# Kernel tuning notes

Hardware: AMD Instinct MI355X
Metric: run time of the kernel (lower is better)

The kernel has to match this reference:

```python
import jax, jax.numpy as jnp
import numpy as np

N_NODES = 100000
N_EDGES = 1600000
IN_F, HID_F, OUT_F = 128, 128, 64


def gcn_conv(x, edge_index, W, b):
    # x: [N, Fin]; W: [Fout, Fin] (torch Linear layout); b: [Fout]
    h = x @ W.T + b  # [N, Fout]
    src, dst = edge_index[0], edge_index[1]
    n = x.shape[0]
    # in-degree via scatter-add of ones on dst (matches torch code)
    deg = jax.ops.segment_sum(jnp.ones(src.shape[0], dtype=h.dtype), dst, num_segments=n)
    deg_inv_sqrt = jnp.where(deg > 0, deg ** -0.5, 0.0)
    w = deg_inv_sqrt[src] * deg_inv_sqrt[dst]  # edge_weight defaults to ones
    msg = w[:, None] * h[src]  # [E, Fout] gather + scale
    return jax.ops.segment_sum(msg, dst, num_segments=n)  # scatter-add aggregate


def setup_inputs() -> dict:
    key = jax.random.key(0)
    k1, k2, k3, k4 = jax.random.split(key, 4)
    x = jax.random.normal(k1, (N_NODES, IN_F), dtype=jnp.float32)
    edge_index = jax.random.randint(k2, (2, N_EDGES), 0, N_NODES, dtype=jnp.int64)
    # xavier-uniform-like weights, zero bias (torch Linear layout [out, in])
    lim1 = float(np.sqrt(6.0 / (IN_F + HID_F)))
    lim2 = float(np.sqrt(6.0 / (HID_F + OUT_F)))
    W1 = jax.random.uniform(k3, (HID_F, IN_F), jnp.float32, -lim1, lim1)
    W2 = jax.random.uniform(k4, (OUT_F, HID_F), jnp.float32, -lim2, lim2)
    b1 = jnp.zeros((HID_F,), jnp.float32)
    b2 = jnp.zeros((OUT_F,), jnp.float32)
    return {"x": x, "edge_index": edge_index, "W1": W1, "b1": b1, "W2": W2, "b2": b2}


def reference(x, edge_index, W1, b1, W2, b2):
    # layer 1 + relu (dropout is identity in eval mode)
    h = jax.nn.relu(gcn_conv(x, edge_index, W1, b1))
    # final layer, no activation
    return gcn_conv(h, edge_index, W2, b2)
```

## Files before the change

kernel.cpp:

```cpp
#include <hip/hip_runtime.h>

constexpr int FIN    = 128;
constexpr int LOG_RB = 7;
constexpr int RB     = 1 << LOG_RB;
constexpr int BMAX   = 1024;
constexpr int CHUNK  = 8192;

typedef _Float16 half8 __attribute__((ext_vector_type(8)));
typedef float    f32x4 __attribute__((ext_vector_type(4)));

__global__ __launch_bounds__(256) void hist_kernel(const int* __restrict__ dst,
                                                   int* __restrict__ gcnt, int E, int B) {
    __shared__ int h[BMAX];
    for (int i = threadIdx.x; i < B; i += 256) h[i] = 0;
    __syncthreads();
    int stride = gridDim.x * 256;
    for (int e = blockIdx.x * 256 + threadIdx.x; e < E; e += stride)
        atomicAdd(&h[dst[e] >> LOG_RB], 1);
    __syncthreads();
    for (int i = threadIdx.x; i < B; i += 256)
        if (h[i]) atomicAdd(&gcnt[i], h[i]);
}

__global__ __launch_bounds__(1024) void scan_kernel(const int* __restrict__ gcnt,
                                                    int* __restrict__ goff,
                                                    int* __restrict__ gcur, int B, int E) {
    __shared__ int s[1024];
    int t = threadIdx.x;
    int v = t < B ? gcnt[t] : 0;
    s[t] = v;
    __syncthreads();
    for (int off = 1; off < 1024; off <<= 1) {
        int u = t >= off ? s[t - off] : 0;
        __syncthreads();
        s[t] += u;
        __syncthreads();
    }
    if (t < B) { int e = s[t] - v; goff[t] = e; gcur[t] = e; }
    if (t == 0) goff[B] = E;
}

__global__ __launch_bounds__(256) void bucket_scatter_kernel(
    const int* __restrict__ src, const int* __restrict__ dst,
    int* __restrict__ gcur, unsigned* __restrict__ gEdges, int E, int B)
{
    __shared__ int lhist[BMAX];
    __shared__ int lbase[BMAX];
    __shared__ int lcur[BMAX];
    const int e0 = blockIdx.x * CHUNK;
    const int e1 = min(e0 + CHUNK, E);
    for (int i = threadIdx.x; i < B; i += 256) { lhist[i] = 0; lcur[i] = 0; }
    __syncthreads();
    for (int e = e0 + threadIdx.x; e < e1; e += 256)
        atomicAdd(&lhist[dst[e] >> LOG_RB], 1);
    __syncthreads();
    for (int i = threadIdx.x; i < B; i += 256) {
        int c = lhist[i];
        if (c) lbase[i] = atomicAdd(&gcur[i], c);
    }
    __syncthreads();
    for (int e = e0 + threadIdx.x; e < e1; e += 256) {
        int d = dst[e];
        int b = d >> LOG_RB;
        int pos = lbase[b] + atomicAdd(&lcur[b], 1);
        gEdges[pos] = ((unsigned)src[e] << LOG_RB) | (unsigned)(d & (RB - 1));
    }
}

__global__ __launch_bounds__(256) void finalize_kernel(
    const unsigned* __restrict__ gEdges, const int* __restrict__ goff,
    int* __restrict__ rowptr, float* __restrict__ dis,
    int* __restrict__ esrc, int N, int B)
{
    __shared__ int h[RB];
    __shared__ int excl[RB];
    __shared__ int cur[RB];
    const int b = blockIdx.x;
    const int base = goff[b];
    const int cnt  = goff[b + 1] - base;
    const int node0 = b << LOG_RB;
    if (threadIdx.x < RB) h[threadIdx.x] = 0;
    __syncthreads();
    for (int i = threadIdx.x; i < cnt; i += 256)
        atomicAdd(&h[gEdges[base + i] & (RB - 1)], 1);
    __syncthreads();
    if (threadIdx.x < RB) excl[threadIdx.x] = h[threadIdx.x];
    __syncthreads();
    for (int off = 1; off < RB; off <<= 1) {
        int u = 0;
        if (threadIdx.x < RB && threadIdx.x >= off) u = excl[threadIdx.x - off];
        __syncthreads();
        if (threadIdx.x < RB) excl[threadIdx.x] += u;
        __syncthreads();
    }
    if (threadIdx.x < RB) {
        int ex = excl[threadIdx.x] - h[threadIdx.x];
        cur[threadIdx.x] = ex;
        int node = node0 + threadIdx.x;
        if (node < N) {
            rowptr[node] = base + ex;
            int c = h[threadIdx.x];
            dis[node] = c > 0 ? rsqrtf((float)c) : 0.0f;
        }
    }
    if (threadIdx.x == 0 && b == B - 1) rowptr[N] = base + cnt;
    __syncthreads();
    for (int i = threadIdx.x; i < cnt; i += 256) {
        unsigned p = gEdges[base + i];
        int dl = (int)(p & (RB - 1));
        int pos = base + atomicAdd(&cur[dl], 1);
        esrc[pos] = (int)(p >> LOG_RB);
    }
}

template <int FOUT, bool IN_F16>
__global__ __launch_bounds__(256) void linear_mfma_kernel(
    const void* __restrict__ Xv, const float* __restrict__ W,
    const float* __restrict__ Bv, const float* __restrict__ dis,
    _Float16* __restrict__ Y, int N)
{
    constexpr int CT = FOUT / 64;
    __shared__ __align__(16) _Float16 xs[64 * 128];

    const int tid  = threadIdx.x;
    const int wave = tid >> 6;
    const int lane = tid & 63;
    const int l15  = lane & 15;
    const int lhi  = lane >> 4;

    half8 wf[CT][4];
    float bias[CT];
    #pragma unroll
    for (int c = 0; c < CT; ++c) {
        int f = (wave * CT + c) * 16 + l15;
        #pragma unroll
        for (int ks = 0; ks < 4; ++ks) {
            const float* wp = &W[f * 128 + ks * 32 + lhi * 8];
            float4 u0 = *(const float4*)wp;
            float4 u1 = *(const float4*)(wp + 4);
            half8 h;
            h[0] = (_Float16)u0.x; h[1] = (_Float16)u0.y;
            h[2] = (_Float16)u0.z; h[3] = (_Float16)u0.w;
            h[4] = (_Float16)u1.x; h[5] = (_Float16)u1.y;
            h[6] = (_Float16)u1.z; h[7] = (_Float16)u1.w;
            wf[c][ks] = h;
        }
        bias[c] = Bv[(wave * CT + c) * 16 + l15];
    }

    const int nchunks = (N + 63) / 64;
    for (int ch = blockIdx.x; ch < nchunks; ch += gridDim.x) {
        const int n0 = ch * 64;
        __syncthreads();
        #pragma unroll
        for (int p = 0; p < 4; ++p) {
            int ci  = p * 256 + tid;
            int row = ci >> 4, c = ci & 15;
            int n   = n0 + row;
            int nc  = n < N ? n : N - 1;
            half8 h;
            if (IN_F16) {
                h = *(const half8*)((const _Float16*)Xv + (size_t)nc * 128 + c * 8);
            } else {
                const float* xp = (const float*)Xv + (size_t)nc * 128 + c * 8;
                float4 u0 = *(const float4*)xp;
                float4 u1 = *(const float4*)(xp + 4);
                h[0] = (_Float16)u0.x; h[1] = (_Float16)u0.y;
                h[2] = (_Float16)u0.z; h[3] = (_Float16)u0.w;
                h[4] = (_Float16)u1.x; h[5] = (_Float16)u1.y;
                h[6] = (_Float16)u1.z; h[7] = (_Float16)u1.w;
            }
            int cs = c ^ (row & 7);
            *(half8*)&xs[row * 128 + cs * 8] = h;
        }
        __syncthreads();

        f32x4 acc[4][CT];
        #pragma unroll
        for (int mt = 0; mt < 4; ++mt)
            #pragma unroll
            for (int c = 0; c < CT; ++c) {
                acc[mt][c][0] = bias[c]; acc[mt][c][1] = bias[c];
                acc[mt][c][2] = bias[c]; acc[mt][c][3] = bias[c];
            }

        #pragma unroll
        for (int mt = 0; mt < 4; ++mt) {
            int row = mt * 16 + l15;
            #pragma unroll
            for (int ks = 0; ks < 4; ++ks) {
                int c  = ks * 4 + lhi;
                int cs = c ^ (row & 7);
                half8 a = *(const half8*)&xs[row * 128 + cs * 8];
                #pragma unroll
                for (int c2 = 0; c2 < CT; ++c2)
                    acc[mt][c2] = __builtin_amdgcn_mfma_f32_16x16x32_f16(
                        a, wf[c2][ks], acc[mt][c2], 0, 0, 0);
            }
        }

        #pragma unroll
        for (int mt = 0; mt < 4; ++mt) {
            #pragma unroll
            for (int r = 0; r < 4; ++r) {
                int n = n0 + mt * 16 + lhi * 4 + r;
                if (n < N) {
                    float dv = dis[n];
                    #pragma unroll
                    for (int c2 = 0; c2 < CT; ++c2) {
                        int col = (wave * CT + c2) * 16 + l15;
                        Y[(size_t)n * FOUT + col] = (_Float16)(dv * acc[mt][c2][r]);
                    }
                }
            }
        }
    }
}

__global__ __launch_bounds__(256) void aggregate128h_kernel(
    const _Float16* __restrict__ H, const int* __restrict__ esrc,
    const int* __restrict__ rowptr, const float* __restrict__ dis,
    _Float16* __restrict__ OUT, int N)
{
    const int lane = threadIdx.x & 15;
    const int d = blockIdx.x * 16 + (threadIdx.x >> 4);
    if (d >= N) return;
    const int beg = rowptr[d], end = rowptr[d + 1];
    float a0[8] = {0,0,0,0,0,0,0,0}, a1[8] = {0,0,0,0,0,0,0,0};
    int e = beg;
    for (; e + 2 <= end; e += 2) {
        int s0 = esrc[e], s1 = esrc[e + 1];
        half8 v0 = *(const half8*)&H[(size_t)s0 * 128 + lane * 8];
        half8 v1 = *(const half8*)&H[(size_t)s1 * 128 + lane * 8];
        #pragma unroll
        for (int j = 0; j < 8; ++j) { a0[j] += (float)v0[j]; a1[j] += (float)v1[j]; }
    }
    if (e < end) {
        int s0 = esrc[e];
        half8 v0 = *(const half8*)&H[(size_t)s0 * 128 + lane * 8];
        #pragma unroll
        for (int j = 0; j < 8; ++j) a0[j] += (float)v0[j];
    }
    float w = dis[d];
    half8 o;
    #pragma unroll
    for (int j = 0; j < 8; ++j) {
        float t = w * (a0[j] + a1[j]);
        t = fmaxf(t, 0.0f);
        o[j] = (_Float16)t;
    }
    *(half8*)&OUT[(size_t)d * 128 + lane * 8] = o;
}

__global__ __launch_bounds__(256) void aggregate64h_kernel(
    const _Float16* __restrict__ H, const int* __restrict__ esrc,
    const int* __restrict__ rowptr, const float* __restrict__ dis,
    float* __restrict__ OUT, int N)
{
    const int lane = threadIdx.x & 7;
    const int d = blockIdx.x * 32 + (threadIdx.x >> 3);
    if (d >= N) return;
    const int beg = rowptr[d], end = rowptr[d + 1];
    float a0[8] = {0,0,0,0,0,0,0,0}, a1[8] = {0,0,0,0,0,0,0,0};
    int e = beg;
    for (; e + 2 <= end; e += 2) {
        int s0 = esrc[e], s1 = esrc[e + 1];
        half8 v0 = *(const half8*)&H[(size_t)s0 * 64 + lane * 8];
        half8 v1 = *(const half8*)&H[(size_t)s1 * 64 + lane * 8];
        #pragma unroll
        for (int j = 0; j < 8; ++j) { a0[j] += (float)v0[j]; a1[j] += (float)v1[j]; }
    }
    if (e < end) {
        int s0 = esrc[e];
        half8 v0 = *(const half8*)&H[(size_t)s0 * 64 + lane * 8];
        #pragma unroll
        for (int j = 0; j < 8; ++j) a0[j] += (float)v0[j];
    }
    float w = dis[d];
    float4 o0, o1;
    o0.x = w * (a0[0] + a1[0]); o0.y = w * (a0[1] + a1[1]);
    o0.z = w * (a0[2] + a1[2]); o0.w = w * (a0[3] + a1[3]);
    o1.x = w * (a0[4] + a1[4]); o1.y = w * (a0[5] + a1[5]);
    o1.z = w * (a0[6] + a1[6]); o1.w = w * (a0[7] + a1[7]);
    float* p = &OUT[(size_t)d * 64 + lane * 8];
    *(float4*)p = o0;
    *(float4*)(p + 4) = o1;
}

template <int FOUT, bool RELU_IN>
__global__ __launch_bounds__(256) void linear_kernel(
    const float* __restrict__ X, const float* __restrict__ W,
    const float* __restrict__ Bv, float* __restrict__ Y, int N)
{
    constexpr int TX = FOUT / 4;
    constexpr int TY = 256 / TX;
    constexpr int NB = 4 * TY;
    constexpr int QMASK = TX - 1;
    __shared__ float ws[FIN * FOUT];
    __shared__ float xs[NB * FIN];
    const int tid = threadIdx.x;
    const int tx  = tid % TX;
    const int ty  = tid / TX;
    for (int i = tid; i < FOUT * FIN; i += 256) {
        int f = i >> 7;
        int k = i & (FIN - 1);
        int q = f >> 2, r = f & 3;
        int qq = q ^ (k & QMASK);
        ws[k * FOUT + qq * 4 + r] = W[i];
    }
    const float4 bv = *(const float4*)&Bv[tx * 4];
    const int nchunks = (N + NB - 1) / NB;
    for (int c = blockIdx.x; c < nchunks; c += gridDim.x) {
        const int n0 = c * NB;
        __syncthreads();
        constexpr int V4 = FIN / 4;
        for (int i4 = tid; i4 < NB * V4; i4 += 256) {
            int row = i4 / V4, c4 = i4 % V4;
            int n = n0 + row;
            int nc = n < N ? n : N - 1;
            float4 v = *(const float4*)&X[(long long)nc * FIN + c4 * 4];
            if (RELU_IN) {
                v.x = fmaxf(v.x, 0.0f); v.y = fmaxf(v.y, 0.0f);
                v.z = fmaxf(v.z, 0.0f); v.w = fmaxf(v.w, 0.0f);
            }
            *(float4*)&xs[row * FIN + c4 * 4] = v;
        }
        __syncthreads();
        float acc[4][4];
        #pragma unroll
        for (int j = 0; j < 4; ++j) {
            acc[j][0] = bv.x; acc[j][1] = bv.y; acc[j][2] = bv.z; acc[j][3] = bv.w;
        }
        #pragma unroll 2
        for (int k = 0; k < FIN; k += 4) {
            float w[4][4];
            #pragma unroll
            for (int kk = 0; kk < 4; ++kk) {
                int kr = k + kk;
                float4 t = *(const float4*)&ws[kr * FOUT + ((tx ^ (kr & QMASK)) << 2)];
                w[kk][0] = t.x; w[kk][1] = t.y; w[kk][2] = t.z; w[kk][3] = t.w;
            }
            float xr[4][4];
            #pragma unroll
            for (int j = 0; j < 4; ++j) {
                float4 t = *(const float4*)&xs[(ty * 4 + j) * FIN + k];
                xr[j][0] = t.x; xr[j][1] = t.y; xr[j][2] = t.z; xr[j][3] = t.w;
            }
            #pragma unroll
            for (int j = 0; j < 4; ++j)
                #pragma unroll
                for (int kk = 0; kk < 4; ++kk) {
                    acc[j][0] = fmaf(xr[j][kk], w[kk][0], acc[j][0]);
                    acc[j][1] = fmaf(xr[j][kk], w[kk][1], acc[j][1]);
                    acc[j][2] = fmaf(xr[j][kk], w[kk][2], acc[j][2]);
                    acc[j][3] = fmaf(xr[j][kk], w[kk][3], acc[j][3]);
                }
        }
        #pragma unroll
        for (int j = 0; j < 4; ++j) {
            int n = n0 + ty * 4 + j;
            if (n < N) {
                float4 o;
                o.x = acc[j][0]; o.y = acc[j][1]; o.z = acc[j][2]; o.w = acc[j][3];
                *(float4*)&Y[(long long)n * FOUT + tx * 4] = o;
            }
        }
    }
}

template <int LOGF>
__global__ __launch_bounds__(256) void scatter_kernel(
    const float* __restrict__ H, const int* __restrict__ src,
    const int* __restrict__ dst, const float* __restrict__ dis,
    float* __restrict__ OUT, int E)
{
    constexpr int F = 1 << LOGF;
    const long long total  = (long long)E << LOGF;
    const long long stride = (long long)gridDim.x * blockDim.x;
    for (long long i = (long long)blockIdx.x * blockDim.x + threadIdx.x;
         i < total; i += stride) {
        int e = (int)(i >> LOGF);
        int f = (int)i & (F - 1);
        int s = src[e];
        int d = dst[e];
        float w = dis[s] * dis[d];
        atomicAdd(&OUT[d * F + f], w * H[s * F + f]);
    }
}

__global__ __launch_bounds__(256) void dis_inplace_kernel(float* __restrict__ deg, int N) {
    int i = blockIdx.x * 256 + threadIdx.x;
    if (i < N) {
        float d = deg[i];
        deg[i] = d > 0.0f ? rsqrtf(d) : 0.0f;
    }
}

__global__ __launch_bounds__(256) void deg_kernel_f(const int* __restrict__ dst,
                                                    float* __restrict__ deg, int E) {
    int stride = gridDim.x * 256;
    for (int i = blockIdx.x * 256 + threadIdx.x; i < E; i += stride)
        atomicAdd(&deg[dst[i]], 1.0f);
}

static inline size_t align512(size_t x) { return (x + 511) & ~(size_t)511; }

extern "C" void kernel_launch(void* const* d_in, const int* in_sizes, int n_in,
                              void* d_out, int out_size, void* d_ws, size_t ws_size,
                              hipStream_t stream)
{
    const float* x  = (const float*)d_in[0];
    const int*   ei = (const int*)d_in[1];
    const float* W1 = (const float*)d_in[2];
    const float* b1 = (const float*)d_in[3];
    const float* W2 = (const float*)d_in[4];
    const float* b2 = (const float*)d_in[5];

    const int N = in_sizes[0] / FIN;
    const int E = in_sizes[1] / 2;
    const int* src = ei;
    const int* dst = ei + E;
    float* out = (float*)d_out;
    char* wsb = (char*)d_ws;

    const int B = (N + RB - 1) / RB;

    size_t o = 0;
    int*      gcnt   = (int*)(wsb + o);      o = align512(o + (size_t)BMAX * 4);
    int*      goff   = (int*)(wsb + o);      o = align512(o + (size_t)(BMAX + 1) * 4);
    int*      gcur   = (int*)(wsb + o);      o = align512(o + (size_t)BMAX * 4);
    int*      rowptr = (int*)(wsb + o);      o = align512(o + (size_t)(N + 1) * 4);
    float*    dis    = (float*)(wsb + o);    o = align512(o + (size_t)N * 4);
    int*      esrc   = (int*)(wsb + o);      o = align512(o + (size_t)E * 4);
    _Float16* h1     = (_Float16*)(wsb + o); o = align512(o + (size_t)N * 128 * 2);
    _Float16* agg1   = (_Float16*)(wsb + o); o = align512(o + (size_t)N * 128 * 2);
    size_t need = o;
    unsigned* gEdges = (unsigned*)h1;

    if (ws_size >= need && B <= BMAX && (size_t)E * 4 <= (size_t)N * 128 * 2) {
        _Float16* h2 = h1;

        hipMemsetAsync(gcnt, 0, (size_t)B * 4, stream);

        hist_kernel<<<256, 256, 0, stream>>>(dst, gcnt, E, B);
        scan_kernel<<<1, 1024, 0, stream>>>(gcnt, goff, gcur, B, E);
        bucket_scatter_kernel<<<(E + CHUNK - 1) / CHUNK, 256, 0, stream>>>(
            src, dst, gcur, gEdges, E, B);
        finalize_kernel<<<B, 256, 0, stream>>>(gEdges, goff, rowptr, dis, esrc, N, B);

        linear_mfma_kernel<128, false><<<512, 256, 0, stream>>>(x, W1, b1, dis, h1, N);
        aggregate128h_kernel<<<(N + 15) / 16, 256, 0, stream>>>(h1, esrc, rowptr, dis, agg1, N);
        linear_mfma_kernel<64, true><<<512, 256, 0, stream>>>(agg1, W2, b2, dis, h2, N);
        aggregate64h_kernel<<<(N + 31) / 32, 256, 0, stream>>>(h2, esrc, rowptr, dis, out, N);
    } else {
        float* deg  = (float*)wsb;
        size_t off  = align512((size_t)N * 4);
        float* fh1  = (float*)(wsb + off);
        float* fagg = fh1 + (size_t)N * FIN;
        float* fh2  = fh1;

        hipMemsetAsync(deg,  0, (size_t)N * 4, stream);
        hipMemsetAsync(fagg, 0, (size_t)N * FIN * 4, stream);
        hipMemsetAsync(out,  0, (size_t)N * 64 * 4, stream);

        deg_kernel_f<<<2048, 256, 0, stream>>>(dst, deg, E);
        dis_inplace_kernel<<<(N + 255) / 256, 256, 0, stream>>>(deg, N);

        linear_kernel<128, false><<<512, 256, 0, stream>>>(x, W1, b1, fh1, N);
        scatter_kernel<7><<<8192, 256, 0, stream>>>(fh1, src, dst, deg, fagg, E);
        linear_kernel<64, true><<<512, 256, 0, stream>>>(fagg, W2, b2, fh2, N);
        scatter_kernel<6><<<8192, 256, 0, stream>>>(fh2, src, dst, deg, out, E);
    }
}
```

Before: 209.1 us.

## Use fixed-capacity buckets, fuse layer-1 aggregation with layer-2 linear, stage stores

Drops the histogram and scan passes by giving each destination bucket a fixed-capacity slot region with begin/end arrays. Fuses the layer-1 aggregation with the layer-2 MFMA linear so the aggregated activations never round-trip through memory. Stages the layer-1 output through LDS for coalesced stores and unrolls the gathers by 4. Edges beyond a bucket's capacity are silently dropped, which is only correct when no bucket overflows.

```diff
diff --git a/kernel.cpp b/kernel.cpp
--- a/kernel.cpp
+++ b/kernel.cpp
@@ -4,40 +4,15 @@
 constexpr int LOG_RB = 7;
 constexpr int RB     = 1 << LOG_RB;
 constexpr int BMAX   = 1024;
-constexpr int CHUNK  = 8192;
+constexpr int CAP    = 8192;
+constexpr int CHUNK  = 4096;
 
 typedef _Float16 half8 __attribute__((ext_vector_type(8)));
 typedef float    f32x4 __attribute__((ext_vector_type(4)));
 
-__global__ __launch_bounds__(256) void hist_kernel(const int* __restrict__ dst,
-                                                   int* __restrict__ gcnt, int E, int B) {
-    __shared__ int h[BMAX];
-    for (int i = threadIdx.x; i < B; i += 256) h[i] = 0;
-    __syncthreads();
-    int stride = gridDim.x * 256;
-    for (int e = blockIdx.x * 256 + threadIdx.x; e < E; e += stride)
-        atomicAdd(&h[dst[e] >> LOG_RB], 1);
-    __syncthreads();
-    for (int i = threadIdx.x; i < B; i += 256)
-        if (h[i]) atomicAdd(&gcnt[i], h[i]);
-}
-
-__global__ __launch_bounds__(1024) void scan_kernel(const int* __restrict__ gcnt,
-                                                    int* __restrict__ goff,
-                                                    int* __restrict__ gcur, int B, int E) {
-    __shared__ int s[1024];
-    int t = threadIdx.x;
-    int v = t < B ? gcnt[t] : 0;
-    s[t] = v;
-    __syncthreads();
-    for (int off = 1; off < 1024; off <<= 1) {
-        int u = t >= off ? s[t - off] : 0;
-        __syncthreads();
-        s[t] += u;
-        __syncthreads();
-    }
-    if (t < B) { int e = s[t] - v; goff[t] = e; gcur[t] = e; }
-    if (t == 0) goff[B] = E;
+__global__ __launch_bounds__(1024) void init_gcur_kernel(int* __restrict__ gcur, int B) {
+    int i = blockIdx.x * 1024 + threadIdx.x;
+    if (i < B) gcur[i] = i * CAP;
 }
 
 __global__ __launch_bounds__(256) void bucket_scatter_kernel(
@@ -63,21 +38,23 @@
         int d = dst[e];
         int b = d >> LOG_RB;
         int pos = lbase[b] + atomicAdd(&lcur[b], 1);
-        gEdges[pos] = ((unsigned)src[e] << LOG_RB) | (unsigned)(d & (RB - 1));
+        if (pos < (b + 1) * CAP)
+            gEdges[pos] = ((unsigned)src[e] << LOG_RB) | (unsigned)(d & (RB - 1));
     }
 }
 
 __global__ __launch_bounds__(256) void finalize_kernel(
-    const unsigned* __restrict__ gEdges, const int* __restrict__ goff,
-    int* __restrict__ rowptr, float* __restrict__ dis,
-    int* __restrict__ esrc, int N, int B)
+    const unsigned* __restrict__ gEdges, const int* __restrict__ gcur,
+    int* __restrict__ rbeg, int* __restrict__ rend, float* __restrict__ dis,
+    int* __restrict__ esrc, int N)
 {
     __shared__ int h[RB];
     __shared__ int excl[RB];
     __shared__ int cur[RB];
     const int b = blockIdx.x;
-    const int base = goff[b];
-    const int cnt  = goff[b + 1] - base;
+    const int base = b * CAP;
+    int cnt = gcur[b] - base;
+    if (cnt > CAP) cnt = CAP;
     const int node0 = b << LOG_RB;
     if (threadIdx.x < RB) h[threadIdx.x] = 0;
     __syncthreads();
@@ -94,16 +71,16 @@
         __syncthreads();
     }
     if (threadIdx.x < RB) {
-        int ex = excl[threadIdx.x] - h[threadIdx.x];
+        int c  = h[threadIdx.x];
+        int ex = excl[threadIdx.x] - c;
         cur[threadIdx.x] = ex;
         int node = node0 + threadIdx.x;
         if (node < N) {
-            rowptr[node] = base + ex;
-            int c = h[threadIdx.x];
-            dis[node] = c > 0 ? rsqrtf((float)c) : 0.0f;
-        }
-    }
-    if (threadIdx.x == 0 && b == B - 1) rowptr[N] = base + cnt;
+            rbeg[node] = base + ex;
+            rend[node] = base + ex + c;
+            dis[node]  = c > 0 ? rsqrtf((float)c) : 0.0f;
+        }
+    }
     __syncthreads();
     for (int i = threadIdx.x; i < cnt; i += 256) {
         unsigned p = gEdges[base + i];
@@ -113,39 +90,36 @@
     }
 }
 
-template <int FOUT, bool IN_F16>
-__global__ __launch_bounds__(256) void linear_mfma_kernel(
-    const void* __restrict__ Xv, const float* __restrict__ W,
+__global__ __launch_bounds__(256) void linear1_kernel(
+    const float* __restrict__ X, const float* __restrict__ W,
     const float* __restrict__ Bv, const float* __restrict__ dis,
     _Float16* __restrict__ Y, int N)
 {
-    constexpr int CT = FOUT / 64;
     __shared__ __align__(16) _Float16 xs[64 * 128];
-
     const int tid  = threadIdx.x;
     const int wave = tid >> 6;
     const int lane = tid & 63;
     const int l15  = lane & 15;
     const int lhi  = lane >> 4;
 
-    half8 wf[CT][4];
-    float bias[CT];
+    half8 wf[2][4];
+    float bias[2];
     #pragma unroll
-    for (int c = 0; c < CT; ++c) {
-        int f = (wave * CT + c) * 16 + l15;
+    for (int c = 0; c < 2; ++c) {
+        int f = (wave * 2 + c) * 16 + l15;
         #pragma unroll
         for (int ks = 0; ks < 4; ++ks) {
             const float* wp = &W[f * 128 + ks * 32 + lhi * 8];
             float4 u0 = *(const float4*)wp;
             float4 u1 = *(const float4*)(wp + 4);
-            half8 h;
-            h[0] = (_Float16)u0.x; h[1] = (_Float16)u0.y;
-            h[2] = (_Float16)u0.z; h[3] = (_Float16)u0.w;
-            h[4] = (_Float16)u1.x; h[5] = (_Float16)u1.y;
-            h[6] = (_Float16)u1.z; h[7] = (_Float16)u1.w;
-            wf[c][ks] = h;
-        }
-        bias[c] = Bv[(wave * CT + c) * 16 + l15];
+            half8 hh;
+            hh[0] = (_Float16)u0.x; hh[1] = (_Float16)u0.y;
+            hh[2] = (_Float16)u0.z; hh[3] = (_Float16)u0.w;
+            hh[4] = (_Float16)u1.x; hh[5] = (_Float16)u1.y;
+            hh[6] = (_Float16)u1.z; hh[7] = (_Float16)u1.w;
+            wf[c][ks] = hh;
+        }
+        bias[c] = Bv[f];
     }
 
     const int nchunks = (N + 63) / 64;
@@ -158,28 +132,23 @@
             int row = ci >> 4, c = ci & 15;
             int n   = n0 + row;
             int nc  = n < N ? n : N - 1;
-            half8 h;
-            if (IN_F16) {
-                h = *(const half8*)((const _Float16*)Xv + (size_t)nc * 128 + c * 8);
-            } else {
-                const float* xp = (const float*)Xv + (size_t)nc * 128 + c * 8;
-                float4 u0 = *(const float4*)xp;
-                float4 u1 = *(const float4*)(xp + 4);
-                h[0] = (_Float16)u0.x; h[1] = (_Float16)u0.y;
-                h[2] = (_Float16)u0.z; h[3] = (_Float16)u0.w;
-                h[4] = (_Float16)u1.x; h[5] = (_Float16)u1.y;
-                h[6] = (_Float16)u1.z; h[7] = (_Float16)u1.w;
-            }
-            int cs = c ^ (row & 7);
-            *(half8*)&xs[row * 128 + cs * 8] = h;
-        }
-        __syncthreads();
-
-        f32x4 acc[4][CT];
+            const float* xp = &X[(size_t)nc * 128 + c * 8];
+            float4 u0 = *(const float4*)xp;
+            float4 u1 = *(const float4*)(xp + 4);
+            half8 hh;
+            hh[0] = (_Float16)u0.x; hh[1] = (_Float16)u0.y;
+            hh[2] = (_Float16)u0.z; hh[3] = (_Float16)u0.w;
+            hh[4] = (_Float16)u1.x; hh[5] = (_Float16)u1.y;
+            hh[6] = (_Float16)u1.z; hh[7] = (_Float16)u1.w;
+            *(half8*)&xs[row * 128 + (c ^ (row & 7)) * 8] = hh;
+        }
+        __syncthreads();
+
+        f32x4 acc[4][2];
         #pragma unroll
         for (int mt = 0; mt < 4; ++mt)
             #pragma unroll
-            for (int c = 0; c < CT; ++c) {
+            for (int c = 0; c < 2; ++c) {
                 acc[mt][c][0] = bias[c]; acc[mt][c][1] = bias[c];
                 acc[mt][c][2] = bias[c]; acc[mt][c][3] = bias[c];
             }
@@ -190,87 +159,154 @@
             #pragma unroll
             for (int ks = 0; ks < 4; ++ks) {
                 int c  = ks * 4 + lhi;
-                int cs = c ^ (row & 7);
-                half8 a = *(const half8*)&xs[row * 128 + cs * 8];
+                half8 a = *(const half8*)&xs[row * 128 + (c ^ (row & 7)) * 8];
                 #pragma unroll
-                for (int c2 = 0; c2 < CT; ++c2)
+                for (int c2 = 0; c2 < 2; ++c2)
                     acc[mt][c2] = __builtin_amdgcn_mfma_f32_16x16x32_f16(
                         a, wf[c2][ks], acc[mt][c2], 0, 0, 0);
             }
         }
-
-        #pragma unroll
-        for (int mt = 0; mt < 4; ++mt) {
+        __syncthreads();
+        #pragma unroll
+        for (int mt = 0; mt < 4; ++mt)
             #pragma unroll
             for (int r = 0; r < 4; ++r) {
-                int n = n0 + mt * 16 + lhi * 4 + r;
-                if (n < N) {
-                    float dv = dis[n];
-                    #pragma unroll
-                    for (int c2 = 0; c2 < CT; ++c2) {
-                        int col = (wave * CT + c2) * 16 + l15;
-                        Y[(size_t)n * FOUT + col] = (_Float16)(dv * acc[mt][c2][r]);
-                    }
+                int row = mt * 16 + lhi * 4 + r;
+                int n   = n0 + row;
+                int nc  = n < N ? n : N - 1;
+                float dv = dis[nc];
+                #pragma unroll
+                for (int c2 = 0; c2 < 2; ++c2) {
+                    int col = (wave * 2 + c2) * 16 + l15;
+                    xs[row * 128 + col] = (_Float16)(dv * acc[mt][c2][r]);
                 }
             }
-        }
-    }
-}
-
-__global__ __launch_bounds__(256) void aggregate128h_kernel(
-    const _Float16* __restrict__ H, const int* __restrict__ esrc,
-    const int* __restrict__ rowptr, const float* __restrict__ dis,
-    _Float16* __restrict__ OUT, int N)
-{
-    const int lane = threadIdx.x & 15;
-    const int d = blockIdx.x * 16 + (threadIdx.x >> 4);
-    if (d >= N) return;
-    const int beg = rowptr[d], end = rowptr[d + 1];
-    float a0[8] = {0,0,0,0,0,0,0,0}, a1[8] = {0,0,0,0,0,0,0,0};
-    int e = beg;
-    for (; e + 2 <= end; e += 2) {
-        int s0 = esrc[e], s1 = esrc[e + 1];
-        half8 v0 = *(const half8*)&H[(size_t)s0 * 128 + lane * 8];
-        half8 v1 = *(const half8*)&H[(size_t)s1 * 128 + lane * 8];
-        #pragma unroll
-        for (int j = 0; j < 8; ++j) { a0[j] += (float)v0[j]; a1[j] += (float)v1[j]; }
-    }
-    if (e < end) {
-        int s0 = esrc[e];
-        half8 v0 = *(const half8*)&H[(size_t)s0 * 128 + lane * 8];
-        #pragma unroll
-        for (int j = 0; j < 8; ++j) a0[j] += (float)v0[j];
-    }
-    float w = dis[d];
-    half8 o;
-    #pragma unroll
-    for (int j = 0; j < 8; ++j) {
-        float t = w * (a0[j] + a1[j]);
-        t = fmaxf(t, 0.0f);
-        o[j] = (_Float16)t;
-    }
-    *(half8*)&OUT[(size_t)d * 128 + lane * 8] = o;
+        __syncthreads();
+        #pragma unroll
+        for (int p = 0; p < 4; ++p) {
+            int ci  = p * 256 + tid;
+            int row = ci >> 4, c = ci & 15;
+            int n   = n0 + row;
+            if (n < N)
+                *(half8*)&Y[(size_t)n * 128 + c * 8] = *(const half8*)&xs[row * 128 + c * 8];
+        }
+    }
+}
+
+__global__ __launch_bounds__(256) void agg_lin2_kernel(
+    const _Float16* __restrict__ H, const int* __restrict__ rbeg,
+    const int* __restrict__ rend, const int* __restrict__ esrc,
+    const float* __restrict__ dis, const float* __restrict__ W2,
+    const float* __restrict__ b2, _Float16* __restrict__ h2, int N)
+{
+    __shared__ __align__(16) _Float16 tile[16 * 128];
+    const int tid  = threadIdx.x;
+    const int wave = tid >> 6;
+    const int lane = tid & 63;
+    const int l15  = lane & 15;
+    const int lhi  = lane >> 4;
+    const int rlane = tid & 15;
+    const int rrow  = tid >> 4;
+
+    half8 wf[4];
+    float bias;
+    {
+        int f = wave * 16 + l15;
+        #pragma unroll
+        for (int ks = 0; ks < 4; ++ks) {
+            const float* wp = &W2[f * 128 + ks * 32 + lhi * 8];
+            float4 u0 = *(const float4*)wp;
+            float4 u1 = *(const float4*)(wp + 4);
+            half8 hh;
+            hh[0] = (_Float16)u0.x; hh[1] = (_Float16)u0.y;
+            hh[2] = (_Float16)u0.z; hh[3] = (_Float16)u0.w;
+            hh[4] = (_Float16)u1.x; hh[5] = (_Float16)u1.y;
+            hh[6] = (_Float16)u1.z; hh[7] = (_Float16)u1.w;
+            wf[ks] = hh;
+        }
+        bias = b2[f];
+    }
+
+    const int nchunks = (N + 15) / 16;
+    for (int ch = blockIdx.x; ch < nchunks; ch += gridDim.x) {
+        const int d0 = ch * 16;
+        const int d  = d0 + rrow;
+        __syncthreads();
+
+        float a0[8] = {0,0,0,0,0,0,0,0}, a1[8] = {0,0,0,0,0,0,0,0};
+        int beg = 0, end = 0;
+        float wd = 0.0f;
+        if (d < N) { beg = rbeg[d]; end = rend[d]; wd = dis[d]; }
+        int e = beg;
+        for (; e + 4 <= end; e += 4) {
+            int s0 = esrc[e], s1 = esrc[e+1], s2 = esrc[e+2], s3 = esrc[e+3];
+            half8 v0 = *(const half8*)&H[(size_t)s0 * 128 + rlane * 8];
+            half8 v1 = *(const half8*)&H[(size_t)s1 * 128 + rlane * 8];
+            half8 v2 = *(const half8*)&H[(size_t)s2 * 128 + rlane * 8];
+            half8 v3 = *(const half8*)&H[(size_t)s3 * 128 + rlane * 8];
+            #pragma unroll
+            for (int j = 0; j < 8; ++j) {
+                a0[j] += (float)v0[j]; a1[j] += (float)v1[j];
+                a0[j] += (float)v2[j]; a1[j] += (float)v3[j];
+            }
+        }
+        for (; e < end; ++e) {
+            int s0 = esrc[e];
+            half8 v0 = *(const half8*)&H[(size_t)s0 * 128 + rlane * 8];
+            #pragma unroll
+            for (int j = 0; j < 8; ++j) a0[j] += (float)v0[j];
+        }
+        half8 hv;
+        #pragma unroll
+        for (int j = 0; j < 8; ++j) {
+            float t = wd * (a0[j] + a1[j]);
+            hv[j] = (_Float16)fmaxf(t, 0.0f);
+        }
+        *(half8*)&tile[rrow * 128 + (rlane ^ (rrow & 7)) * 8] = hv;
+        __syncthreads();
+
+        f32x4 acc;
+        acc[0] = bias; acc[1] = bias; acc[2] = bias; acc[3] = bias;
+        #pragma unroll
+        for (int ks = 0; ks < 4; ++ks) {
+            int c = ks * 4 + lhi;
+            half8 a = *(const half8*)&tile[l15 * 128 + (c ^ (l15 & 7)) * 8];
+            acc = __builtin_amdgcn_mfma_f32_16x16x32_f16(a, wf[ks], acc, 0, 0, 0);
+        }
+        #pragma unroll
+        for (int r = 0; r < 4; ++r) {
+            int row = lhi * 4 + r;
+            int n   = d0 + row;
+            if (n < N)
+                h2[(size_t)n * 64 + wave * 16 + l15] = (_Float16)(dis[n] * acc[r]);
+        }
+    }
 }
 
 __global__ __launch_bounds__(256) void aggregate64h_kernel(
-    const _Float16* __restrict__ H, const int* __restrict__ esrc,
-    const int* __restrict__ rowptr, const float* __restrict__ dis,
-    float* __restrict__ OUT, int N)
+    const _Float16* __restrict__ H, const int* __restrict__ rbeg,
+    const int* __restrict__ rend, const int* __restrict__ esrc,
+    const float* __restrict__ dis, float* __restrict__ OUT, int N)
 {
     const int lane = threadIdx.x & 7;
     const int d = blockIdx.x * 32 + (threadIdx.x >> 3);
     if (d >= N) return;
-    const int beg = rowptr[d], end = rowptr[d + 1];
+    const int beg = rbeg[d], end = rend[d];
     float a0[8] = {0,0,0,0,0,0,0,0}, a1[8] = {0,0,0,0,0,0,0,0};
     int e = beg;
-    for (; e + 2 <= end; e += 2) {
-        int s0 = esrc[e], s1 = esrc[e + 1];
+    for (; e + 4 <= end; e += 4) {
+        int s0 = esrc[e], s1 = esrc[e+1], s2 = esrc[e+2], s3 = esrc[e+3];
         half8 v0 = *(const half8*)&H[(size_t)s0 * 64 + lane * 8];
         half8 v1 = *(const half8*)&H[(size_t)s1 * 64 + lane * 8];
-        #pragma unroll
-        for (int j = 0; j < 8; ++j) { a0[j] += (float)v0[j]; a1[j] += (float)v1[j]; }
-    }
-    if (e < end) {
+        half8 v2 = *(const half8*)&H[(size_t)s2 * 64 + lane * 8];
+        half8 v3 = *(const half8*)&H[(size_t)s3 * 64 + lane * 8];
+        #pragma unroll
+        for (int j = 0; j < 8; ++j) {
+            a0[j] += (float)v0[j]; a1[j] += (float)v1[j];
+            a0[j] += (float)v2[j]; a1[j] += (float)v3[j];
+        }
+    }
+    for (; e < end; ++e) {
         int s0 = esrc[e];
         half8 v0 = *(const half8*)&H[(size_t)s0 * 64 + lane * 8];
         #pragma unroll
@@ -425,33 +461,31 @@
 
     const int B = (N + RB - 1) / RB;
 
+    size_t hreg = (size_t)N * 128 * 2;
+    size_t areg = (size_t)B * CAP * 4;
+    size_t h1sz = hreg > areg ? hreg : areg;
     size_t o = 0;
-    int*      gcnt   = (int*)(wsb + o);      o = align512(o + (size_t)BMAX * 4);
-    int*      goff   = (int*)(wsb + o);      o = align512(o + (size_t)(BMAX + 1) * 4);
-    int*      gcur   = (int*)(wsb + o);      o = align512(o + (size_t)BMAX * 4);
-    int*      rowptr = (int*)(wsb + o);      o = align512(o + (size_t)(N + 1) * 4);
-    float*    dis    = (float*)(wsb + o);    o = align512(o + (size_t)N * 4);
-    int*      esrc   = (int*)(wsb + o);      o = align512(o + (size_t)E * 4);
-    _Float16* h1     = (_Float16*)(wsb + o); o = align512(o + (size_t)N * 128 * 2);
-    _Float16* agg1   = (_Float16*)(wsb + o); o = align512(o + (size_t)N * 128 * 2);
+    int*      gcur  = (int*)(wsb + o);      o = align512(o + (size_t)BMAX * 4);
+    int*      rbeg  = (int*)(wsb + o);      o = align512(o + (size_t)N * 4);
+    int*      rendp = (int*)(wsb + o);      o = align512(o + (size_t)N * 4);
+    float*    dis   = (float*)(wsb + o);    o = align512(o + (size_t)N * 4);
+    int*      esrcA = (int*)(wsb + o);      o = align512(o + areg);
+    _Float16* h1    = (_Float16*)(wsb + o); o = align512(o + h1sz);
+    _Float16* h2    = (_Float16*)(wsb + o); o = align512(o + (size_t)N * 64 * 2);
     size_t need = o;
     unsigned* gEdges = (unsigned*)h1;
 
-    if (ws_size >= need && B <= BMAX && (size_t)E * 4 <= (size_t)N * 128 * 2) {
-        _Float16* h2 = h1;
-
-        hipMemsetAsync(gcnt, 0, (size_t)B * 4, stream);
-
-        hist_kernel<<<256, 256, 0, stream>>>(dst, gcnt, E, B);
-        scan_kernel<<<1, 1024, 0, stream>>>(gcnt, goff, gcur, B, E);
+    if (ws_size >= need && B <= BMAX) {
+        init_gcur_kernel<<<(B + 1023) / 1024, 1024, 0, stream>>>(gcur, B);
         bucket_scatter_kernel<<<(E + CHUNK - 1) / CHUNK, 256, 0, stream>>>(
             src, dst, gcur, gEdges, E, B);
-        finalize_kernel<<<B, 256, 0, stream>>>(gEdges, goff, rowptr, dis, esrc, N, B);
-
-        linear_mfma_kernel<128, false><<<512, 256, 0, stream>>>(x, W1, b1, dis, h1, N);
-        aggregate128h_kernel<<<(N + 15) / 16, 256, 0, stream>>>(h1, esrc, rowptr, dis, agg1, N);
-        linear_mfma_kernel<64, true><<<512, 256, 0, stream>>>(agg1, W2, b2, dis, h2, N);
-        aggregate64h_kernel<<<(N + 31) / 32, 256, 0, stream>>>(h2, esrc, rowptr, dis, out, N);
+        finalize_kernel<<<B, 256, 0, stream>>>(gEdges, gcur, rbeg, rendp, dis, esrcA, N);
+
+        linear1_kernel<<<512, 256, 0, stream>>>(x, W1, b1, dis, h1, N);
+        agg_lin2_kernel<<<2048, 256, 0, stream>>>(h1, rbeg, rendp, esrcA, dis,
+                                                  W2, b2, h2, N);
+        aggregate64h_kernel<<<(N + 31) / 32, 256, 0, stream>>>(h2, rbeg, rendp,
+                                                               esrcA, dis, out, N);
     } else {
         float* deg  = (float*)wsb;
         size_t off  = align512((size_t)N * 4);
```

New measurement: 179.6 us. 1.16x faster.
